# Performance work log

Measured on AMD Instinct MI355X. Metric: run time of the kernel, lower is better.

## Reference

```python
import jax, jax.numpy as jnp
import numpy as np

EMBED_DIM = 768
NUM_HEADS = 12
HEAD_DIM = EMBED_DIM // NUM_HEADS  # 64
B, N = 2, 3073
SCALE = HEAD_DIM ** -0.5


def setup_inputs() -> dict:
    key = jax.random.key(0)
    ks = jax.random.split(key, 6)
    s = EMBED_DIM ** -0.5
    return {
        "x": jax.random.normal(ks[0], (B, N, EMBED_DIM), dtype=jnp.float32),
        "qkv_w": jax.random.normal(ks[1], (3 * EMBED_DIM, EMBED_DIM), dtype=jnp.float32) * s,
        "proj_w": jax.random.normal(ks[2], (EMBED_DIM, EMBED_DIM), dtype=jnp.float32) * s,
        "proj_b": jax.random.normal(ks[3], (EMBED_DIM,), dtype=jnp.float32) * 0.02,
        "conv_w": jax.random.normal(ks[4], (HEAD_DIM, 1, 3, 3), dtype=jnp.float32) * 0.02,
        "conv_b": jax.random.normal(ks[5], (HEAD_DIM,), dtype=jnp.float32) * 0.02,
    }


def _local_pos_embed(v, conv_w, conv_b):
    # v: [B, H, N, C] with C = head_dim; drop cls token, fold to spatial grid
    b, h, n, c = v.shape
    u = int(((n - 1) // 12) ** 0.5)
    Hh, Ww = 4 * u, 3 * u
    xs = jnp.transpose(v[:, :, 1:], (0, 1, 3, 2)).reshape(b * h, c, Hh, Ww)
    pe = jax.lax.conv_general_dilated(
        xs, conv_w, window_strides=(1, 1), padding=((1, 1), (1, 1)),
        feature_group_count=c, dimension_numbers=("NCHW", "OIHW", "NCHW"))
    pe = pe + conv_b[None, :, None, None]
    pe = pe.reshape(b, h, c, n - 1).transpose(0, 1, 3, 2)  # [B,H,N-1,C]
    zeros = jnp.zeros((b, h, 1, c), dtype=pe.dtype)
    return jnp.concatenate([zeros, pe], axis=2)  # [B,H,N,C]


def reference(x, qkv_w, proj_w, proj_b, conv_w, conv_b):
    b, n, d = x.shape
    qkv = x @ qkv_w.T  # [B, N, 3D]
    qkv = qkv.reshape(b, n, 3, NUM_HEADS, HEAD_DIM).transpose(2, 0, 3, 1, 4)  # [3,B,H,N,Dh]
    q, k, v = qkv[0], qkv[1], qkv[2]
    scores = jnp.einsum("bhqd,bhkd->bhqk", q, k) * SCALE
    attn = jax.nn.softmax(scores, axis=-1)
    out = jnp.einsum("bham,bhmv->bhav", attn, v)  # [B,H,N,Dh]
    out = out + _local_pos_embed(v, conv_w, conv_b)
    out = out.transpose(0, 2, 1, 3).reshape(b, n, d)  # b h n d -> b n (h d)
    return out @ proj_w.T + proj_b
```

## Files before the change

kernel.cpp:

```cpp
#include <hip/hip_runtime.h>
#include <math.h>

#define NB 2
#define SEQ 3073
#define DIM 768
#define NH 12
#define DH 64
#define HHH 64
#define WWW 48
#define NPATCH 3072
#define QSCALE_L2E 0.18033688f
#define KSPLIT 1536

#define BHN (NB * NH)
#define MROWS (NB * SEQ)
#define MPAD 6272
#define CNT (BHN * SEQ * DH)
#define VTSTRIDE 3136

typedef __attribute__((ext_vector_type(8))) short s8v;
typedef __attribute__((ext_vector_type(4))) float f4v;
typedef __attribute__((ext_vector_type(4))) ushort u4v;

#define MFMA16(a, b, c) __builtin_amdgcn_mfma_f32_16x16x32_bf16((a), (b), (c), 0, 0, 0)

__device__ __forceinline__ ushort f2bf(float f) {
    unsigned x = __float_as_uint(f);
    return (ushort)((x + 0x7FFFu + ((x >> 16) & 1u)) >> 16);
}
__device__ __forceinline__ float bf2f(ushort u) {
    return __uint_as_float(((unsigned)u) << 16);
}
__device__ __forceinline__ unsigned cvt_pk_bf16(float a, float b) {
    unsigned r;
    asm("v_cvt_pk_bf16_f32 %0, %1, %2" : "=v"(r) : "v"(a), "v"(b));
    return r;
}
__device__ __forceinline__ void gl_lds16(const ushort* g, ushort* l) {
    __builtin_amdgcn_global_load_lds(
        (const __attribute__((address_space(1))) unsigned int*)g,
        (__attribute__((address_space(3))) unsigned int*)l, 16, 0, 0);
}

__device__ __forceinline__ s8v ldsFrag(const ushort* base, int row, int half, int t) {
    int byte = (row * 128 + half * 64 + t * 16) ^ ((row & 7) << 4);
    return *(const s8v*)((const char*)base + byte);
}

__global__ __launch_bounds__(256) void cast_bf16(const float* __restrict__ in,
                                                 ushort* __restrict__ out,
                                                 int n_in, int n_grp) {
    for (int g = blockIdx.x * 256 + threadIdx.x; g < n_grp; g += gridDim.x * 256) {
        int i0 = g * 4;
        float4 vv;
        if (i0 + 4 <= n_in) {
            vv = *(const float4*)(in + i0);
        } else {
            vv.x = (i0 + 0 < n_in) ? in[i0 + 0] : 0.f;
            vv.y = (i0 + 1 < n_in) ? in[i0 + 1] : 0.f;
            vv.z = (i0 + 2 < n_in) ? in[i0 + 2] : 0.f;
            vv.w = (i0 + 3 < n_in) ? in[i0 + 3] : 0.f;
        }
        u4v hv;
        hv[0] = f2bf(vv.x); hv[1] = f2bf(vv.y);
        hv[2] = f2bf(vv.z); hv[3] = f2bf(vv.w);
        *(u4v*)(out + i0) = hv;
    }
}

__device__ __forceinline__ void mfma_tile_768_s1(const ushort* __restrict__ gA,
                                                 const ushort* __restrict__ gB,
                                                 ushort* Ah, ushort* Bh,
                                                 f4v acc[4][4]) {
    const int tid = threadIdx.x;
    const int lane = tid & 63;
    const int w = tid >> 6;
    const int lo = lane & 15, t = lane >> 4;
    const int wr = w >> 1, wc = w & 1;
    const int w4 = w * 4;

    for (int k0 = 0; k0 < DIM; k0 += 64) {
        __syncthreads();
        #pragma unroll
        for (int i = 0; i < 4; ++i) {
            int s = (w4 + i) * 64 + lane;
            int r = s >> 3, c = s & 7;
            int cp = c ^ (r & 7);
            size_t go = (size_t)r * DIM + k0 + cp * 8;
            int lb = (w4 + i) * 1024;
            gl_lds16(gA + go, (ushort*)((char*)Ah + lb));
            gl_lds16(gB + go, (ushort*)((char*)Bh + lb));
        }
        __syncthreads();

        #pragma unroll
        for (int h = 0; h < 2; ++h) {
            s8v af[4];
            #pragma unroll
            for (int i = 0; i < 4; ++i)
                af[i] = ldsFrag(Ah, wr * 64 + i * 16 + lo, h, t);
            #pragma unroll
            for (int j = 0; j < 4; ++j) {
                s8v bf = ldsFrag(Bh, wc * 64 + j * 16 + lo, h, t);
                #pragma unroll
                for (int i = 0; i < 4; ++i)
                    acc[i][j] = MFMA16(af[i], bf, acc[i][j]);
            }
        }
    }
}

__global__ __launch_bounds__(256) void qkv_mfma(const ushort* __restrict__ xh,
                                                const ushort* __restrict__ wh,
                                                ushort* __restrict__ q_bf,
                                                ushort* __restrict__ k_bf,
                                                ushort* __restrict__ v_bf,
                                                ushort* __restrict__ vt) {
    __shared__ __align__(16) ushort Ah[8192], Bh[8192];
    const int m0 = blockIdx.x * 128;
    const int nb = blockIdx.y;
    f4v acc[4][4] = {};
    mfma_tile_768_s1(xh + (size_t)m0 * DIM,
                     wh + (size_t)nb * 128 * DIM, Ah, Bh, acc);

    const int tid = threadIdx.x;
    const int lane = tid & 63;
    const int w = tid >> 6;
    const int lo = lane & 15, t = lane >> 4;
    const int wr = w >> 1, wc = w & 1;
    const int which = nb / 6;
    const int rr0 = (nb % 6) * 128;

    #pragma unroll
    for (int i = 0; i < 4; ++i) {
        #pragma unroll
        for (int r = 0; r < 4; ++r) {
            int m = m0 + wr * 64 + i * 16 + t * 4 + r;
            if (m >= MROWS) continue;
            int bb = m / SEQ;
            int row = m - bb * SEQ;
            #pragma unroll
            for (int j = 0; j < 4; ++j) {
                int rr = rr0 + wc * 64 + j * 16 + lo;
                int hh = rr >> 6, dd = rr & 63;
                size_t base = ((size_t)(bb * NH + hh) * SEQ + row) * DH + dd;
                float val = acc[i][j][r];
                if (which == 0) {
                    q_bf[base] = f2bf(val * QSCALE_L2E);
                } else if (which == 1) {
                    k_bf[base] = f2bf(val);
                } else {
                    ushort vb = f2bf(val);
                    v_bf[base] = vb;
                    vt[((size_t)(bb * NH + hh) * DH + dd) * VTSTRIDE + row] = vb;
                }
            }
        }
    }
}

__global__ __launch_bounds__(256) void proj_mfma(const ushort* __restrict__ ah,
                                                 const ushort* __restrict__ pwh,
                                                 const float* __restrict__ bias,
                                                 float* __restrict__ out) {
    __shared__ __align__(16) ushort Ah[8192], Bh[8192];
    const int m0 = blockIdx.x * 128;
    const int nb = blockIdx.y;
    f4v acc[4][4] = {};
    mfma_tile_768_s1(ah + (size_t)m0 * DIM,
                     pwh + (size_t)nb * 128 * DIM, Ah, Bh, acc);

    const int tid = threadIdx.x;
    const int lane = tid & 63;
    const int w = tid >> 6;
    const int lo = lane & 15, t = lane >> 4;
    const int wr = w >> 1, wc = w & 1;

    #pragma unroll
    for (int i = 0; i < 4; ++i) {
        #pragma unroll
        for (int r = 0; r < 4; ++r) {
            int m = m0 + wr * 64 + i * 16 + t * 4 + r;
            if (m >= MROWS) continue;
            #pragma unroll
            for (int j = 0; j < 4; ++j) {
                int n = nb * 128 + wc * 64 + j * 16 + lo;
                out[(size_t)m * DIM + n] = acc[i][j][r] + bias[n];
            }
        }
    }
}

__global__ __launch_bounds__(128, 2) void attn_mfma(const ushort* __restrict__ qh,
                                                    const ushort* __restrict__ kh,
                                                    const ushort* __restrict__ vt,
                                                    float* __restrict__ o0,
                                                    float* __restrict__ o1,
                                                    float* __restrict__ pli) {
    __shared__ __align__(16) ushort Kh[4096];
    __shared__ __align__(16) ushort Vt[5120];
    __shared__ __align__(16) ushort Pl[2][2048];

    const int tid = threadIdx.x;
    const int w = tid >> 6;
    const int lane = tid & 63;
    const int lo = lane & 15;
    const int t = lane >> 4;
    const int bh = blockIdx.y;
    const int q0 = blockIdx.x * 64;
    const int z = blockIdx.z;
    const int kbeg = z * KSPLIT;
    const int kend = z ? SEQ : KSPLIT;

    {
        int rr = 64 + (tid >> 3);
        int col = (tid & 7) * 8;
        int byte = (rr * 128 + col * 2) ^ ((rr & 7) << 4);
        short v = (rr == 64) ? (short)0x3F80 : (short)0;
        s8v ones = {v, v, v, v, v, v, v, v};
        *(s8v*)((char*)Vt + byte) = ones;
    }

    s8v qf0[2], qf1[2];
    #pragma unroll
    for (int g = 0; g < 2; ++g) {
        int qr = q0 + w * 32 + g * 16 + lo;
        if (qr > SEQ - 1) qr = SEQ - 1;
        const size_t qoff = ((size_t)bh * SEQ + qr) * DH + t * 8;
        qf0[g] = *(const s8v*)(qh + qoff);
        qf1[g] = *(const s8v*)(qh + qoff + 32);
    }

    const int rr = tid >> 1;
    const int cc = (tid & 1) * 4;
    int sbyte[4];
    #pragma unroll
    for (int i = 0; i < 4; ++i)
        sbyte[i] = (rr * 128 + (cc + i) * 16) ^ ((rr & 7) << 4);
    const ushort* gk = kh + (size_t)bh * SEQ * DH;
    const ushort* gvb = vt + (size_t)bh * DH * VTSTRIDE;

    s8v pkh[4], pvv[4];
    #pragma unroll
    for (int i = 0; i < 4; ++i) {
        pkh[i] = *(const s8v*)(gk + (size_t)(kbeg + rr) * DH + (cc + i) * 8);
        pvv[i] = *(const s8v*)(gvb + (size_t)rr * VTSTRIDE + kbeg + (cc + i) * 8);
    }

    f4v o[2][5] = {};

    for (int k0 = kbeg; k0 < kend; k0 += 64) {
        #pragma unroll
        for (int i = 0; i < 4; ++i) {
            *(s8v*)((char*)Kh + sbyte[i]) = pkh[i];
            *(s8v*)((char*)Vt + sbyte[i]) = pvv[i];
        }
        __syncthreads();

        const int kn = k0 + 64;
        if (kn < SEQ) {
            #pragma unroll
            for (int i = 0; i < 4; ++i) {
                pkh[i] = *(const s8v*)(gk + (size_t)(kn + rr) * DH + (cc + i) * 8);
                pvv[i] = *(const s8v*)(gvb + (size_t)rr * VTSTRIDE + kn + (cc + i) * 8);
            }
        }

        f4v sv[2][4];
        __builtin_amdgcn_s_setprio(1);
        #pragma unroll
        for (int tc = 0; tc < 4; ++tc) {
            int row = tc * 16 + lo;
            s8v b0 = ldsFrag(Kh, row, 0, t);
            s8v b1 = ldsFrag(Kh, row, 1, t);
            #pragma unroll
            for (int g = 0; g < 2; ++g) {
                f4v a = {0.f, 0.f, 0.f, 0.f};
                a = MFMA16(b0, qf0[g], a);
                a = MFMA16(b1, qf1[g], a);
                sv[g][tc] = a;
            }
        }
        __builtin_amdgcn_s_setprio(0);

        if (k0 + 64 > SEQ) {
            #pragma unroll
            for (int tc = 0; tc < 4; ++tc)
                #pragma unroll
                for (int r = 0; r < 4; ++r)
                    if (k0 + tc * 16 + 4 * t + r >= SEQ) {
                        sv[0][tc][r] = -1e30f;
                        sv[1][tc][r] = -1e30f;
                    }
        }

        #pragma unroll
        for (int g = 0; g < 2; ++g) {
            int prow = g * 16 + lo;
            int rb = prow * 128 + t * 8;
            #pragma unroll
            for (int tc = 0; tc < 4; ++tc) {
                float p0 = exp2f(sv[g][tc][0]);
                float p1 = exp2f(sv[g][tc][1]);
                float p2 = exp2f(sv[g][tc][2]);
                float p3 = exp2f(sv[g][tc][3]);
                uint2 pk;
                pk.x = cvt_pk_bf16(p0, p1);
                pk.y = cvt_pk_bf16(p2, p3);
                int byte = (rb + tc * 32) ^ ((lo & 7) << 4);
                *(uint2*)((char*)Pl[w] + byte) = pk;
            }
        }

        s8v pf0[2], pf1[2];
        #pragma unroll
        for (int g = 0; g < 2; ++g) {
            pf0[g] = ldsFrag(Pl[w], g * 16 + lo, 0, t);
            pf1[g] = ldsFrag(Pl[w], g * 16 + lo, 1, t);
        }
        __builtin_amdgcn_s_setprio(1);
        #pragma unroll
        for (int dt = 0; dt < 5; ++dt) {
            s8v v0 = ldsFrag(Vt, dt * 16 + lo, 0, t);
            s8v v1 = ldsFrag(Vt, dt * 16 + lo, 1, t);
            #pragma unroll
            for (int g = 0; g < 2; ++g) {
                o[g][dt] = MFMA16(pf0[g], v0, o[g][dt]);
                o[g][dt] = MFMA16(pf1[g], v1, o[g][dt]);
            }
        }
        __builtin_amdgcn_s_setprio(0);

        __syncthreads();
    }

    const int b = bh / NH;
    const int h = bh - b * NH;
    float* obase = z ? o1 : o0;
    float* lbase = pli + (size_t)z * BHN * SEQ;
    #pragma unroll
    for (int g = 0; g < 2; ++g) {
        #pragma unroll
        for (int r = 0; r < 4; ++r) {
            int row = q0 + w * 32 + g * 16 + t * 4 + r;
            if (row >= SEQ) continue;
            if (lo == 0)
                lbase[(size_t)bh * SEQ + row] = o[g][4][r];
            #pragma unroll
            for (int dt = 0; dt < 4; ++dt)
                obase[((size_t)(b * SEQ + row)) * DIM + h * DH + dt * 16 + lo] =
                    o[g][dt][r];
        }
    }
}

__global__ __launch_bounds__(256) void conv_pe(const ushort* __restrict__ v,
                                               const float* __restrict__ cw,
                                               const float* __restrict__ cb,
                                               ushort* __restrict__ pe) {
    const int tid = threadIdx.x;
    const int c = tid & 63;
    const int tl = tid >> 6;
    const int blk = blockIdx.x;
    const int bh = blk / 768;
    const int pb = blk - bh * 768;
    const int p = pb * 4 + tl;
    const int y = p / WWW;
    const int x0 = p - y * WWW;

    const ushort* vb = v + (size_t)bh * SEQ * DH;
    float acc = cb[c];
    #pragma unroll
    for (int dy = -1; dy <= 1; ++dy) {
        int yy = y + dy;
        if (yy < 0 || yy >= HHH) continue;
        #pragma unroll
        for (int dx = -1; dx <= 1; ++dx) {
            int xx = x0 + dx;
            if (xx < 0 || xx >= WWW) continue;
            acc = fmaf(bf2f(vb[(size_t)(1 + yy * WWW + xx) * DH + c]),
                       cw[c * 9 + (dy + 1) * 3 + (dx + 1)], acc);
        }
    }
    const int b = bh / NH;
    const int h = bh - b * NH;
    pe[((size_t)(b * SEQ + 1 + p)) * DIM + h * DH + c] = f2bf(acc);
}

__global__ __launch_bounds__(256) void combine_att(const float* __restrict__ o0,
                                                   const float* __restrict__ o1,
                                                   const float* __restrict__ pli,
                                                   const ushort* __restrict__ pe,
                                                   ushort* __restrict__ ah) {
    const int total = MROWS * DIM / 4;
    for (int i = blockIdx.x * 256 + threadIdx.x; i < total; i += gridDim.x * 256) {
        size_t e = (size_t)i * 4;
        int m = (int)(e / DIM);
        int d = (int)(e - (size_t)m * DIM);
        int b = m / SEQ;
        int row = m - b * SEQ;
        int h = d >> 6;
        size_t li = (size_t)(b * NH + h) * SEQ + row;
        float inv = 1.f / (pli[li] + pli[(size_t)BHN * SEQ + li]);
        float4 a = *(const float4*)(o0 + e);
        float4 p = *(const float4*)(o1 + e);
        float pv[4] = {0.f, 0.f, 0.f, 0.f};
        if (row > 0) {
            u4v pb = *(const u4v*)(pe + e);
            #pragma unroll
            for (int j = 0; j < 4; ++j) pv[j] = bf2f(pb[j]);
        }
        u4v rs;
        rs[0] = f2bf(fmaf(a.x + p.x, inv, pv[0]));
        rs[1] = f2bf(fmaf(a.y + p.y, inv, pv[1]));
        rs[2] = f2bf(fmaf(a.z + p.z, inv, pv[2]));
        rs[3] = f2bf(fmaf(a.w + p.w, inv, pv[3]));
        *(u4v*)(ah + e) = rs;
    }
}

extern "C" void kernel_launch(void* const* d_in, const int* in_sizes, int n_in,
                              void* d_out, int out_size, void* d_ws, size_t ws_size,
                              hipStream_t stream) {
    const float* x      = (const float*)d_in[0];
    const float* qkv_w  = (const float*)d_in[1];
    const float* proj_w = (const float*)d_in[2];
    const float* proj_b = (const float*)d_in[3];
    const float* conv_w = (const float*)d_in[4];
    const float* conv_b = (const float*)d_in[5];
    float* out = (float*)d_out;

    ushort* ws = (ushort*)d_ws;
    size_t o = 0;
    ushort* xh  = ws + o; o += (size_t)MPAD * DIM;
    o += (size_t)MPAD * DIM;
    ushort* wh  = ws + o; o += (size_t)2304 * DIM;
    ushort* pwh = ws + o; o += (size_t)DIM * DIM;
    ushort* q_bf = ws + o; o += CNT;
    ushort* k_bf = ws + o; o += CNT;
    ushort* v_bf = ws + o; o += CNT;
    ushort* vtb  = ws + o; o += (size_t)BHN * DH * VTSTRIDE;
    float*  o0   = (float*)(ws + o);
    float*  po1 = (float*)ws;
    float*  pli = (float*)(ws + (size_t)MROWS * DIM * 2);
    ushort* pe  = vtb;
    ushort* ah  = q_bf;

    cast_bf16<<<2048, 256, 0, stream>>>(x, xh, MROWS * DIM, MPAD * DIM / 4);
    cast_bf16<<<1024, 256, 0, stream>>>(qkv_w, wh, 2304 * DIM, 2304 * DIM / 4);
    cast_bf16<<<512, 256, 0, stream>>>(proj_w, pwh, DIM * DIM, DIM * DIM / 4);

    qkv_mfma<<<dim3(49, 18), 256, 0, stream>>>(xh, wh, q_bf, k_bf, v_bf, vtb);
    attn_mfma<<<dim3(49, BHN, 2), 128, 0, stream>>>(q_bf, k_bf, vtb, o0, po1, pli);
    conv_pe<<<BHN * (NPATCH / 4), 256, 0, stream>>>(v_bf, conv_w, conv_b, pe);
    combine_att<<<2048, 256, 0, stream>>>(o0, po1, pli, pe, ah);
    proj_mfma<<<dim3(49, 6), 256, 0, stream>>>(ah, pwh, proj_b, out);
}
```

Baseline: 245.7 us.

## Double attention query tile per block and compute softmax row sums in registers

Each wave now handles 64 query rows instead of 32, so a block covers 128 queries and the grid halves. Every K/V tile staged in LDS is therefore reused by twice as many queries. The row sum of the softmax is now accumulated in registers and reduced across lanes with shuffles, replacing the extra MFMA column against a row of ones in V. This drops a fifth of the PV MFMAs, but it raises register pressure and doubles the P buffer in LDS, which may lower occupancy. With only 25x24x2 blocks, the grid may also fill the GPU less evenly.

```diff
diff --git a/kernel.cpp b/kernel.cpp
--- a/kernel.cpp
+++ b/kernel.cpp
@@ -198,8 +198,8 @@
                                                     float* __restrict__ o1,
                                                     float* __restrict__ pli) {
     __shared__ __align__(16) ushort Kh[4096];
-    __shared__ __align__(16) ushort Vt[5120];
-    __shared__ __align__(16) ushort Pl[2][2048];
+    __shared__ __align__(16) ushort Vt[4096];
+    __shared__ __align__(16) ushort Pl[2][4096];
 
     const int tid = threadIdx.x;
     const int w = tid >> 6;
@@ -207,24 +207,15 @@
     const int lo = lane & 15;
     const int t = lane >> 4;
     const int bh = blockIdx.y;
-    const int q0 = blockIdx.x * 64;
+    const int q0 = blockIdx.x * 128;
     const int z = blockIdx.z;
     const int kbeg = z * KSPLIT;
     const int kend = z ? SEQ : KSPLIT;
 
-    {
-        int rr = 64 + (tid >> 3);
-        int col = (tid & 7) * 8;
-        int byte = (rr * 128 + col * 2) ^ ((rr & 7) << 4);
-        short v = (rr == 64) ? (short)0x3F80 : (short)0;
-        s8v ones = {v, v, v, v, v, v, v, v};
-        *(s8v*)((char*)Vt + byte) = ones;
-    }
-
-    s8v qf0[2], qf1[2];
-    #pragma unroll
-    for (int g = 0; g < 2; ++g) {
-        int qr = q0 + w * 32 + g * 16 + lo;
+    s8v qf0[4], qf1[4];
+    #pragma unroll
+    for (int g = 0; g < 4; ++g) {
+        int qr = q0 + w * 64 + g * 16 + lo;
         if (qr > SEQ - 1) qr = SEQ - 1;
         const size_t qoff = ((size_t)bh * SEQ + qr) * DH + t * 8;
         qf0[g] = *(const s8v*)(qh + qoff);
@@ -247,7 +238,8 @@
         pvv[i] = *(const s8v*)(gvb + (size_t)rr * VTSTRIDE + kbeg + (cc + i) * 8);
     }
 
-    f4v o[2][5] = {};
+    f4v o[4][4] = {};
+    float lp[4] = {0.f, 0.f, 0.f, 0.f};
 
     for (int k0 = kbeg; k0 < kend; k0 += 64) {
         #pragma unroll
@@ -266,65 +258,49 @@
             }
         }
 
-        f4v sv[2][4];
-        __builtin_amdgcn_s_setprio(1);
+        const bool tail = (k0 + 64 > SEQ);
         #pragma unroll
         for (int tc = 0; tc < 4; ++tc) {
             int row = tc * 16 + lo;
             s8v b0 = ldsFrag(Kh, row, 0, t);
             s8v b1 = ldsFrag(Kh, row, 1, t);
             #pragma unroll
-            for (int g = 0; g < 2; ++g) {
+            for (int g = 0; g < 4; ++g) {
                 f4v a = {0.f, 0.f, 0.f, 0.f};
                 a = MFMA16(b0, qf0[g], a);
                 a = MFMA16(b1, qf1[g], a);
-                sv[g][tc] = a;
-            }
-        }
-        __builtin_amdgcn_s_setprio(0);
-
-        if (k0 + 64 > SEQ) {
-            #pragma unroll
-            for (int tc = 0; tc < 4; ++tc)
-                #pragma unroll
-                for (int r = 0; r < 4; ++r)
-                    if (k0 + tc * 16 + 4 * t + r >= SEQ) {
-                        sv[0][tc][r] = -1e30f;
-                        sv[1][tc][r] = -1e30f;
-                    }
-        }
-
-        #pragma unroll
-        for (int g = 0; g < 2; ++g) {
-            int prow = g * 16 + lo;
-            int rb = prow * 128 + t * 8;
-            #pragma unroll
-            for (int tc = 0; tc < 4; ++tc) {
-                float p0 = exp2f(sv[g][tc][0]);
-                float p1 = exp2f(sv[g][tc][1]);
-                float p2 = exp2f(sv[g][tc][2]);
-                float p3 = exp2f(sv[g][tc][3]);
+                if (tail) {
+                    #pragma unroll
+                    for (int r = 0; r < 4; ++r)
+                        if (k0 + tc * 16 + 4 * t + r >= SEQ) a[r] = -1e30f;
+                }
+                float p0 = exp2f(a[0]);
+                float p1 = exp2f(a[1]);
+                float p2 = exp2f(a[2]);
+                float p3 = exp2f(a[3]);
+                lp[g] += (p0 + p1) + (p2 + p3);
                 uint2 pk;
                 pk.x = cvt_pk_bf16(p0, p1);
                 pk.y = cvt_pk_bf16(p2, p3);
-                int byte = (rb + tc * 32) ^ ((lo & 7) << 4);
+                int prow = g * 16 + lo;
+                int byte = (prow * 128 + t * 8 + tc * 32) ^ ((lo & 7) << 4);
                 *(uint2*)((char*)Pl[w] + byte) = pk;
             }
         }
 
-        s8v pf0[2], pf1[2];
-        #pragma unroll
-        for (int g = 0; g < 2; ++g) {
+        s8v pf0[4], pf1[4];
+        #pragma unroll
+        for (int g = 0; g < 4; ++g) {
             pf0[g] = ldsFrag(Pl[w], g * 16 + lo, 0, t);
             pf1[g] = ldsFrag(Pl[w], g * 16 + lo, 1, t);
         }
         __builtin_amdgcn_s_setprio(1);
         #pragma unroll
-        for (int dt = 0; dt < 5; ++dt) {
+        for (int dt = 0; dt < 4; ++dt) {
             s8v v0 = ldsFrag(Vt, dt * 16 + lo, 0, t);
             s8v v1 = ldsFrag(Vt, dt * 16 + lo, 1, t);
             #pragma unroll
-            for (int g = 0; g < 2; ++g) {
+            for (int g = 0; g < 4; ++g) {
                 o[g][dt] = MFMA16(pf0[g], v0, o[g][dt]);
                 o[g][dt] = MFMA16(pf1[g], v1, o[g][dt]);
             }
@@ -332,6 +308,12 @@
         __builtin_amdgcn_s_setprio(0);
 
         __syncthreads();
+    }
+
+    #pragma unroll
+    for (int g = 0; g < 4; ++g) {
+        lp[g] += __shfl_xor(lp[g], 16);
+        lp[g] += __shfl_xor(lp[g], 32);
     }
 
     const int b = bh / NH;
@@ -339,13 +321,16 @@
     float* obase = z ? o1 : o0;
     float* lbase = pli + (size_t)z * BHN * SEQ;
     #pragma unroll
-    for (int g = 0; g < 2; ++g) {
+    for (int g = 0; g < 4; ++g) {
+        if (t == 0) {
+            int row = q0 + w * 64 + g * 16 + lo;
+            if (row < SEQ)
+                lbase[(size_t)bh * SEQ + row] = lp[g];
+        }
         #pragma unroll
         for (int r = 0; r < 4; ++r) {
-            int row = q0 + w * 32 + g * 16 + t * 4 + r;
+            int row = q0 + w * 64 + g * 16 + t * 4 + r;
             if (row >= SEQ) continue;
-            if (lo == 0)
-                lbase[(size_t)bh * SEQ + row] = o[g][4][r];
             #pragma unroll
             for (int dt = 0; dt < 4; ++dt)
                 obase[((size_t)(b * SEQ + row)) * DIM + h * DH + dt * 16 + lo] =
@@ -451,7 +436,7 @@
     cast_bf16<<<512, 256, 0, stream>>>(proj_w, pwh, DIM * DIM, DIM * DIM / 4);
 
     qkv_mfma<<<dim3(49, 18), 256, 0, stream>>>(xh, wh, q_bf, k_bf, v_bf, vtb);
-    attn_mfma<<<dim3(49, BHN, 2), 128, 0, stream>>>(q_bf, k_bf, vtb, o0, po1, pli);
+    attn_mfma<<<dim3(25, BHN, 2), 128, 0, stream>>>(q_bf, k_bf, vtb, o0, po1, pli);
     conv_pe<<<BHN * (NPATCH / 4), 256, 0, stream>>>(v_bf, conv_w, conv_b, pe);
     combine_att<<<2048, 256, 0, stream>>>(o0, po1, pli, pe, ah);
     proj_mfma<<<dim3(49, 6), 256, 0, stream>>>(ah, pwh, proj_b, out);
```

New measurement: 272.8 us. 1.11x slower.
